# Kernel optimization log

Measured on AMD Instinct MI355X. Metric: run time of the kernel, lower is better.

## Reference

```python
import jax, jax.numpy as jnp
import numpy as np
import math

N_HEAD = 16
N_KV_HEAD = 4
N_EMBD = 2048
HEAD_DIM = N_EMBD // N_HEAD  # 128
SCALE = 1.0 / math.sqrt(HEAD_DIM)
B, T = 2, 2048


def setup_inputs() -> dict:
    key = jax.random.key(0)
    ks = jax.random.split(key, 5)
    s = 0.02
    x = jax.random.normal(ks[0], (B, T, N_EMBD), dtype=jnp.float32)
    wq = jax.random.normal(ks[1], (N_EMBD, N_EMBD), dtype=jnp.float32) * s
    wk = jax.random.normal(ks[2], (N_KV_HEAD * HEAD_DIM, N_EMBD), dtype=jnp.float32) * s
    wv = jax.random.normal(ks[3], (N_KV_HEAD * HEAD_DIM, N_EMBD), dtype=jnp.float32) * s
    wo = jax.random.normal(ks[4], (N_EMBD, N_EMBD), dtype=jnp.float32) * s
    return {"x": x, "wq": wq, "wk": wk, "wv": wv, "wo": wo}


def _forward(x, wq, wk, wv, wo):
    b, t, _ = x.shape
    # Linear layers: y = x @ W.T  (torch Linear weight is (out,in))
    q = (x @ wq.T).reshape(b, t, N_HEAD, HEAD_DIM).transpose(0, 2, 1, 3)      # (B,H,T,D)
    k = (x @ wk.T).reshape(b, t, N_KV_HEAD, HEAD_DIM).transpose(0, 2, 1, 3)  # (B,Hkv,T,D)
    v = (x @ wv.T).reshape(b, t, N_KV_HEAD, HEAD_DIM).transpose(0, 2, 1, 3)
    groups = N_HEAD // N_KV_HEAD
    k = jnp.repeat(k, groups, axis=1)  # repeat_interleave over head dim -> (B,H,T,D)
    v = jnp.repeat(v, groups, axis=1)
    # Causal mask: True above diagonal (masked-out positions)
    mask = jnp.triu(jnp.ones((t, t), dtype=bool), k=1)[None, None]  # (1,1,T,T)
    scores = jnp.einsum('bhqd,bhkd->bhqk', q, k) * SCALE
    scores = jnp.where(mask, -jnp.inf, scores)
    attn = jax.nn.softmax(scores, axis=-1)
    attn = jnp.where(mask, 0.0, attn)
    y = jnp.einsum('bhqk,bhkd->bhqd', attn, v)       # (B,H,T,D)
    y = y.transpose(0, 2, 1, 3).reshape(b, t, N_EMBD)
    return y @ wo.T


def reference(x, wq, wk, wv, wo):
    return _forward(x, wq, wk, wv, wo)
```

## Files before the change

### kernel.cpp

```cpp
#include <hip/hip_runtime.h>
#include <cstdint>
#include <cstddef>

typedef __bf16 bf16_t;
typedef __bf16 bf16x8 __attribute__((ext_vector_type(8)));
typedef __bf16 bf16x4 __attribute__((ext_vector_type(4)));
typedef float f32x4 __attribute__((ext_vector_type(4)));

#define GL2LDS16(gptr, lptr)                                                   \
  __builtin_amdgcn_global_load_lds(                                            \
      (__attribute__((address_space(1))) void*)(gptr),                         \
      (__attribute__((address_space(3))) void*)(lptr), 16, 0, 0)

__device__ __forceinline__ float fast_exp2(float x) {
  float r;
  asm volatile("v_exp_f32 %0, %1" : "=v"(r) : "v"(x));
  return r;
}

#define BATCH 2
#define T_SEQ 2048
#define NH 16
#define NKV 4
#define HD 128
#define EMB 2048
#define KVDIM (NKV * HD)
#define MROWS (BATCH * T_SEQ)

__global__ void cvt_all(const float4* __restrict__ x,  const float4* __restrict__ wq,
                        const float4* __restrict__ wk, const float4* __restrict__ wv,
                        const float4* __restrict__ wo,
                        bf16x4* __restrict__ xb,  bf16x4* __restrict__ wqb,
                        bf16x4* __restrict__ wkb, bf16x4* __restrict__ wvb,
                        bf16x4* __restrict__ wob) {
  const int blk = blockIdx.x;
  const float4* src;
  bf16x4* dst;
  int base;
  if (blk < 8192)       { src = x;  dst = xb;  base = blk; }
  else if (blk < 12288) { src = wq; dst = wqb; base = blk - 8192; }
  else if (blk < 13312) { src = wk; dst = wkb; base = blk - 12288; }
  else if (blk < 14336) { src = wv; dst = wvb; base = blk - 13312; }
  else                  { src = wo; dst = wob; base = blk - 14336; }
  const int i = base * 256 + threadIdx.x;
  const float4 v = src[i];
  dst[i] = bf16x4{(__bf16)v.x, (__bf16)v.y, (__bf16)v.z, (__bf16)v.w};
}

#define BK8 64
#define NT8 (EMB / BK8)

#define LDA(dst, buf, half)                                                    \
  _Pragma("unroll")                                                            \
  for (int i_ = 0; i_ < 4; ++i_) {                                             \
    const int row_ = wm + (half) * 64 + i_ * 16 + l15;                         \
    _Pragma("unroll")                                                          \
    for (int ks_ = 0; ks_ < 2; ++ks_)                                          \
      dst[i_][ks_] = *(const bf16x8*)&(buf)[row_ * 64 +                        \
                                            (((ks_ * 4 + lq) ^ (row_ & 7)) * 8)]; \
  }

#define LDB(dst, buf, qoff)                                                    \
  _Pragma("unroll")                                                            \
  for (int j_ = 0; j_ < 2; ++j_) {                                             \
    const int row_ = 256 + wn + (qoff) + j_ * 16 + l15;                        \
    _Pragma("unroll")                                                          \
    for (int ks_ = 0; ks_ < 2; ++ks_)                                          \
      dst[j_][ks_] = *(const bf16x8*)&(buf)[row_ * 64 +                        \
                                            (((ks_ * 4 + lq) ^ (row_ & 7)) * 8)]; \
  }

#define MM(Af, Bf, ai, bj)                                                     \
  __builtin_amdgcn_s_setprio(1);                                               \
  _Pragma("unroll")                                                            \
  for (int ks_ = 0; ks_ < 2; ++ks_)                                            \
    _Pragma("unroll")                                                          \
    for (int i_ = 0; i_ < 4; ++i_)                                             \
      _Pragma("unroll")                                                        \
      for (int j_ = 0; j_ < 2; ++j_)                                           \
        acc[(ai) + i_][(bj) + j_] = __builtin_amdgcn_mfma_f32_16x16x32_bf16(   \
            Af[i_][ks_], Bf[j_][ks_], acc[(ai) + i_][(bj) + j_], 0, 0, 0);     \
  __builtin_amdgcn_s_setprio(0);

__global__ __launch_bounds__(512, 2)
void gemm_qkv8(const bf16_t* __restrict__ A,
               const bf16_t* __restrict__ Wq, const bf16_t* __restrict__ Wk,
               const bf16_t* __restrict__ Wv,
               bf16_t* __restrict__ Qb, bf16_t* __restrict__ Kb,
               bf16_t* __restrict__ Vt, float qalpha)
{
  __shared__ bf16_t lds0[512 * 64];
  __shared__ bf16_t lds1[512 * 64];

  const int tid  = threadIdx.x;
  const int lane = tid & 63;
  const int wv   = tid >> 6;
  const int l15  = lane & 15;
  const int lq   = lane >> 4;

  const int bid0 = blockIdx.x;
  const int bid  = (bid0 & 7) * 24 + (bid0 >> 3);
  const int mt = bid / 12, nt = bid % 12;
  const int m0 = mt * 256;

  const bf16_t* Bmat; int ncol0, seg;
  if (nt < 8)       { Bmat = Wq; ncol0 = nt * 256;        seg = 0; }
  else if (nt < 10) { Bmat = Wk; ncol0 = (nt - 8) * 256;  seg = 1; }
  else              { Bmat = Wv; ncol0 = (nt - 10) * 256; seg = 2; }

  const int wm = (wv >> 2) * 128;
  const int wn = (wv & 3) * 64;

  f32x4 acc[8][4] = {};

  auto stageAll = [&](bf16_t* dstbuf, int tsrc) {
    const int k0 = tsrc * BK8;
#pragma unroll
    for (int h = 0; h < 4; ++h) {
      const bf16_t* src = (h < 2) ? A : Bmat;
      const int rbase = (h < 2) ? (m0 + h * 128) : (ncol0 + (h - 2) * 128);
      bf16_t* dst = dstbuf + h * 8192;
#pragma unroll
      for (int r = 0; r < 2; ++r) {
        const int c = r * 512 + tid;
        const int row = c >> 3, p = c & 7;
        const int sb = p ^ (row & 7);
        GL2LDS16(src + (size_t)(rbase + row) * EMB + k0 + sb * 8, dst + c * 8);
      }
    }
  };

  stageAll(lds0, 0);
  stageAll(lds1, 1);
  asm volatile("s_waitcnt vmcnt(8)" ::: "memory");
  __builtin_amdgcn_s_barrier();

  bf16x8 a03[4][2], a47[4][2], b01[2][2], b23[2][2];
  LDA(a03, lds0, 0);
  LDB(b01, lds0, 0);

#pragma unroll 1
  for (int t = 0; t < NT8; ++t) {
    bf16_t* curb = (t & 1) ? lds1 : lds0;
    bf16_t* nxtb = (t & 1) ? lds0 : lds1;
    const int tn2 = (t + 2 < NT8) ? t + 2 : NT8 - 1;

    LDB(b23, curb, 32);
    MM(a03, b01, 0, 0);
    __builtin_amdgcn_s_barrier();

    LDA(a47, curb, 1);
    MM(a03, b23, 0, 2);
    asm volatile("s_waitcnt vmcnt(0)" ::: "memory");
    __builtin_amdgcn_s_barrier();

    LDA(a03, nxtb, 0);
    MM(a47, b01, 4, 0);
    __builtin_amdgcn_s_barrier();

    stageAll(curb, tn2);
    LDB(b01, nxtb, 0);
    MM(a47, b23, 4, 2);
    __builtin_amdgcn_s_barrier();
  }
  asm volatile("s_waitcnt vmcnt(0)" ::: "memory");

  if (seg == 0) {
#pragma unroll
    for (int i = 0; i < 8; ++i) {
      const int rbase = m0 + wm + i * 16 + lq * 4;
#pragma unroll
      for (int j = 0; j < 4; ++j) {
        const int col = ncol0 + wn + j * 16 + l15;
#pragma unroll
        for (int r = 0; r < 4; ++r)
          Qb[(size_t)(rbase + r) * EMB + col] = (bf16_t)(acc[i][j][r] * qalpha);
      }
    }
  } else if (seg == 1) {
#pragma unroll
    for (int i = 0; i < 8; ++i) {
      const int rbase = m0 + wm + i * 16 + lq * 4;
#pragma unroll
      for (int j = 0; j < 4; ++j) {
        const int col = ncol0 + wn + j * 16 + l15;
#pragma unroll
        for (int r = 0; r < 4; ++r)
          Kb[(size_t)(rbase + r) * KVDIM + col] = (bf16_t)acc[i][j][r];
      }
    }
  } else {
    const int bb = m0 >> 11;
    const int mloc0 = (m0 & 2047) + wm + lq * 4;
#pragma unroll
    for (int i = 0; i < 8; ++i) {
      const int mloc = mloc0 + i * 16;
#pragma unroll
      for (int j = 0; j < 4; ++j) {
        const int d = ncol0 + wn + j * 16 + l15;
        *(bf16x4*)(Vt + (size_t)(bb * KVDIM + d) * T_SEQ + mloc) =
            bf16x4{(__bf16)acc[i][j][0], (__bf16)acc[i][j][1],
                   (__bf16)acc[i][j][2], (__bf16)acc[i][j][3]};
      }
    }
  }
}

__global__ __launch_bounds__(256, 2)
void gemm_out(const bf16_t* __restrict__ A, const bf16_t* __restrict__ Bm,
              float* __restrict__ C, int M, int N, int K)
{
  __shared__ bf16_t As[128 * 64];
  __shared__ bf16_t Bs[128 * 64];

  const int tid  = threadIdx.x;
  const int lane = tid & 63;
  const int wv   = tid >> 6;
  const int m0 = blockIdx.y * 128;
  const int n0 = blockIdx.x * 128;
  const int wm = (wv >> 1) * 64;
  const int wn = (wv & 1) * 64;
  const int l15 = lane & 15;
  const int lq  = lane >> 4;

  f32x4 acc[4][4] = {};
  const int srow = tid >> 3;
  const int scol = (tid & 7) * 8;

  for (int k0 = 0; k0 < K; k0 += 64) {
#pragma unroll
    for (int r = 0; r < 4; ++r) {
      const int row = r * 32 + srow;
      GL2LDS16(A + (size_t)(m0 + row) * K + k0 + scol, As + row * 64 + scol);
    }
#pragma unroll
    for (int r = 0; r < 4; ++r) {
      const int row = r * 32 + srow;
      GL2LDS16(Bm + (size_t)(n0 + row) * K + k0 + scol, Bs + row * 64 + scol);
    }
    __syncthreads();

#pragma unroll
    for (int ks = 0; ks < 2; ++ks) {
      const int kc = ks * 32 + lq * 8;
      bf16x8 af[4], bf[4];
#pragma unroll
      for (int i = 0; i < 4; ++i)
        af[i] = *(const bf16x8*)(As + (wm + i * 16 + l15) * 64 + kc);
#pragma unroll
      for (int j = 0; j < 4; ++j)
        bf[j] = *(const bf16x8*)(Bs + (wn + j * 16 + l15) * 64 + kc);
#pragma unroll
      for (int i = 0; i < 4; ++i)
#pragma unroll
        for (int j = 0; j < 4; ++j)
          acc[i][j] = __builtin_amdgcn_mfma_f32_16x16x32_bf16(af[i], bf[j], acc[i][j], 0, 0, 0);
    }
    __syncthreads();
  }

#pragma unroll
  for (int i = 0; i < 4; ++i) {
    const int rbase = m0 + wm + i * 16 + lq * 4;
#pragma unroll
    for (int j = 0; j < 4; ++j) {
      const int col = n0 + wn + j * 16 + l15;
#pragma unroll
      for (int r = 0; r < 4; ++r)
        C[(size_t)(rbase + r) * N + col] = acc[i][j][r];
    }
  }
}

#define PSTR 72

__global__ __launch_bounds__(256, 2)
void attn_fwd(const bf16_t* __restrict__ Q, const bf16_t* __restrict__ Kg,
              const bf16_t* __restrict__ Vt, bf16_t* __restrict__ Y)
{
  __shared__ bf16_t Ks[2][64 * 128];
  __shared__ bf16_t Vs[2][128 * 64];
  __shared__ bf16_t Ps[4][16 * PSTR];

  const int tid  = threadIdx.x;
  const int lane = tid & 63;
  const int wv   = tid >> 6;
  const int l15  = lane & 15;
  const int lq   = lane >> 4;
  const int h  = blockIdx.y;
  const int b  = blockIdx.z;
  const int hkv = h >> 2;
  bf16_t* Psw = Ps[wv];

  auto stage = [&](int kt, int bufsel) {
    const int base_t = b * T_SEQ + kt * 64;
#pragma unroll
    for (int r = 0; r < 4; ++r) {
      const int c = r * 256 + tid;
      const int row = c >> 4, p = c & 15;
      const int sb = p ^ (row & 7);
      GL2LDS16(Kg + (size_t)(base_t + row) * KVDIM + hkv * HD + sb * 8,
               &Ks[bufsel][c * 8]);
    }
#pragma unroll
    for (int r = 0; r < 4; ++r) {
      const int c = r * 256 + tid;
      const int row = c >> 3, p = c & 7;
      const int sb = p ^ (row & 7);
      GL2LDS16(Vt + (size_t)(b * KVDIM + hkv * HD + row) * T_SEQ + kt * 64 + sb * 8,
               &Vs[bufsel][c * 8]);
    }
  };

#pragma unroll 1
  for (int ph = 0; ph < 2; ++ph) {
    const int qt = ph ? blockIdx.x : (31 - blockIdx.x);
    const int q0 = qt * 64;
    const int nkt = qt + 1;
    const int qabs = q0 + wv * 16 + l15;

    bf16x8 qf[4];
    {
      const bf16_t* qp = Q + ((size_t)(b * T_SEQ + qabs) * NH + h) * HD + lq * 8;
#pragma unroll
      for (int ds = 0; ds < 4; ++ds)
        qf[ds] = *(const bf16x8*)(qp + ds * 32);
    }

    float l_part = 0.f;
    f32x4 o[8];
#pragma unroll
    for (int nb = 0; nb < 8; ++nb) o[nb] = f32x4{0.f, 0.f, 0.f, 0.f};

    __syncthreads();
    stage(0, 0);

    for (int kt = 0; kt < nkt; ++kt) {
      const int cur = kt & 1;
      __syncthreads();
      if (kt + 1 < nkt) stage(kt + 1, cur ^ 1);

      f32x4 s[4];
#pragma unroll
      for (int nb = 0; nb < 4; ++nb) {
        s[nb] = f32x4{0.f, 0.f, 0.f, 0.f};
        const int row = nb * 16 + l15;
        const int r7  = row & 7;
#pragma unroll
        for (int ds = 0; ds < 4; ++ds) {
          const bf16x8 kf = *(const bf16x8*)&Ks[cur][row * 128 + (((ds * 4 + lq) ^ r7) * 8)];
          s[nb] = __builtin_amdgcn_mfma_f32_16x16x32_bf16(kf, qf[ds], s[nb], 0, 0, 0);
        }
      }

      const bool dia = (kt == nkt - 1);
#pragma unroll
      for (int nb = 0; nb < 4; ++nb) {
        const int kvb = kt * 64 + nb * 16 + lq * 4;
        float p0, p1, p2, p3;
        if (dia) {
          p0 = (kvb + 0 <= qabs) ? fast_exp2(s[nb][0]) : 0.f;
          p1 = (kvb + 1 <= qabs) ? fast_exp2(s[nb][1]) : 0.f;
          p2 = (kvb + 2 <= qabs) ? fast_exp2(s[nb][2]) : 0.f;
          p3 = (kvb + 3 <= qabs) ? fast_exp2(s[nb][3]) : 0.f;
        } else {
          p0 = fast_exp2(s[nb][0]);
          p1 = fast_exp2(s[nb][1]);
          p2 = fast_exp2(s[nb][2]);
          p3 = fast_exp2(s[nb][3]);
        }
        l_part += (p0 + p1) + (p2 + p3);
        *(bf16x4*)(Psw + l15 * PSTR + nb * 16 + lq * 4) =
            bf16x4{(__bf16)p0, (__bf16)p1, (__bf16)p2, (__bf16)p3};
      }

      asm volatile("s_waitcnt lgkmcnt(0)" ::: "memory");

#pragma unroll
      for (int ks = 0; ks < 2; ++ks) {
        const bf16x8 pf = *(const bf16x8*)(Psw + l15 * PSTR + ks * 32 + lq * 8);
#pragma unroll
        for (int nb = 0; nb < 8; ++nb) {
          const int row = nb * 16 + l15;
          const bf16x8 vf = *(const bf16x8*)&Vs[cur][row * 64 + (((ks * 4 + lq) ^ (row & 7)) * 8)];
          o[nb] = __builtin_amdgcn_mfma_f32_16x16x32_bf16(vf, pf, o[nb], 0, 0, 0);
        }
      }
    }

    float lt = l_part;
    lt += __shfl_xor(lt, 16);
    lt += __shfl_xor(lt, 32);
    const float inv = 1.f / lt;
    bf16_t* yp = Y + ((size_t)(b * T_SEQ + qabs) * NH + h) * HD + lq * 4;
#pragma unroll
    for (int nb = 0; nb < 8; ++nb) {
      *(bf16x4*)(yp + nb * 16) = bf16x4{(__bf16)(o[nb][0] * inv), (__bf16)(o[nb][1] * inv),
                                        (__bf16)(o[nb][2] * inv), (__bf16)(o[nb][3] * inv)};
    }
  }
}

extern "C" void kernel_launch(void* const* d_in, const int* in_sizes, int n_in,
                              void* d_out, int out_size, void* d_ws, size_t ws_size,
                              hipStream_t stream) {
  const float* x  = (const float*)d_in[0];
  const float* wq = (const float*)d_in[1];
  const float* wk = (const float*)d_in[2];
  const float* wv = (const float*)d_in[3];
  const float* wo = (const float*)d_in[4];
  float* out = (float*)d_out;

  const size_t n_x  = (size_t)MROWS * EMB;
  const size_t n_wq = (size_t)EMB * EMB;
  const size_t n_wk = (size_t)KVDIM * EMB;

  bf16_t* xb  = (bf16_t*)d_ws;
  bf16_t* wqb = xb  + n_x;
  bf16_t* wkb = wqb + n_wq;
  bf16_t* wvb = wkb + n_wk;
  bf16_t* wob = wvb + n_wk;
  bf16_t* Qb  = wob + n_wq;
  bf16_t* Kb  = Qb + (size_t)MROWS * EMB;
  bf16_t* Vtb = Kb + (size_t)MROWS * KVDIM;
  bf16_t* Yb  = Vtb + (size_t)MROWS * KVDIM;

  dim3 blk(256);

  cvt_all<<<dim3(18432), blk, 0, stream>>>(
      (const float4*)x, (const float4*)wq, (const float4*)wk, (const float4*)wv, (const float4*)wo,
      (bf16x4*)xb, (bf16x4*)wqb, (bf16x4*)wkb, (bf16x4*)wvb, (bf16x4*)wob);

  const float qalpha = 0.08838834764831845f * 1.4426950408889634f;
  gemm_qkv8<<<dim3(192), dim3(512), 0, stream>>>(xb, wqb, wkb, wvb,
                                                 Qb, Kb, Vtb, qalpha);

  attn_fwd<<<dim3(16, NH, BATCH), blk, 0, stream>>>(Qb, Kb, Vtb, Yb);

  gemm_out<<<dim3(EMB / 128, MROWS / 128), blk, 0, stream>>>(Yb, wob, out, MROWS, EMB, EMB);
}
```

Before: 282.4 us.

## Retile fused QKV GEMM to 256x192 tiles for 256 blocks

The fused QKV projection GEMM moves from 256x256 tiles (192 blocks) to 256x192 tiles (256 blocks), so the 3072-wide output splits into 16 column tiles that can straddle the Q/K/V boundaries. This is meant to fill all 256 compute units on the MI355X instead of leaving a quarter idle. Per-chunk weight-row selection is added for loads and per-16-column selection for stores, and the LDS staging and MFMA schedule are reworked with finer-grained half-A and B prefetches. The cost is lower arithmetic intensity per block and more barriers per k-step.

```diff
diff --git a/kernel.cpp b/kernel.cpp
--- a/kernel.cpp
+++ b/kernel.cpp
@@ -49,6 +49,7 @@
 
 #define BK8 64
 #define NT8 (EMB / BK8)
+#define BN 192
 
 #define LDA(dst, buf, half)                                                    \
   _Pragma("unroll")                                                            \
@@ -60,17 +61,26 @@
                                             (((ks_ * 4 + lq) ^ (row_ & 7)) * 8)]; \
   }
 
-#define LDB(dst, buf, qoff)                                                    \
+#define LDB2(dst, buf)                                                         \
   _Pragma("unroll")                                                            \
   for (int j_ = 0; j_ < 2; ++j_) {                                             \
-    const int row_ = 256 + wn + (qoff) + j_ * 16 + l15;                        \
+    const int row_ = 256 + wn + j_ * 16 + l15;                                 \
     _Pragma("unroll")                                                          \
     for (int ks_ = 0; ks_ < 2; ++ks_)                                          \
       dst[j_][ks_] = *(const bf16x8*)&(buf)[row_ * 64 +                        \
                                             (((ks_ * 4 + lq) ^ (row_ & 7)) * 8)]; \
   }
 
-#define MM(Af, Bf, ai, bj)                                                     \
+#define LDB1(dst, buf)                                                         \
+  {                                                                            \
+    const int row_ = 256 + wn + 32 + l15;                                      \
+    _Pragma("unroll")                                                          \
+    for (int ks_ = 0; ks_ < 2; ++ks_)                                          \
+      dst[ks_] = *(const bf16x8*)&(buf)[row_ * 64 +                            \
+                                        (((ks_ * 4 + lq) ^ (row_ & 7)) * 8)];  \
+  }
+
+#define MM16(Af, Bf, ai)                                                       \
   __builtin_amdgcn_s_setprio(1);                                               \
   _Pragma("unroll")                                                            \
   for (int ks_ = 0; ks_ < 2; ++ks_)                                            \
@@ -78,8 +88,18 @@
     for (int i_ = 0; i_ < 4; ++i_)                                             \
       _Pragma("unroll")                                                        \
       for (int j_ = 0; j_ < 2; ++j_)                                           \
-        acc[(ai) + i_][(bj) + j_] = __builtin_amdgcn_mfma_f32_16x16x32_bf16(   \
-            Af[i_][ks_], Bf[j_][ks_], acc[(ai) + i_][(bj) + j_], 0, 0, 0);     \
+        acc[(ai) + i_][j_] = __builtin_amdgcn_mfma_f32_16x16x32_bf16(          \
+            Af[i_][ks_], Bf[j_][ks_], acc[(ai) + i_][j_], 0, 0, 0);            \
+  __builtin_amdgcn_s_setprio(0);
+
+#define MM8(Af, Bf, ai)                                                        \
+  __builtin_amdgcn_s_setprio(1);                                               \
+  _Pragma("unroll")                                                            \
+  for (int ks_ = 0; ks_ < 2; ++ks_)                                            \
+    _Pragma("unroll")                                                          \
+    for (int i_ = 0; i_ < 4; ++i_)                                             \
+      acc[(ai) + i_][2] = __builtin_amdgcn_mfma_f32_16x16x32_bf16(             \
+          Af[i_][ks_], Bf[ks_], acc[(ai) + i_][2], 0, 0, 0);                   \
   __builtin_amdgcn_s_setprio(0);
 
 __global__ __launch_bounds__(512, 2)
@@ -89,8 +109,8 @@
                bf16_t* __restrict__ Qb, bf16_t* __restrict__ Kb,
                bf16_t* __restrict__ Vt, float qalpha)
 {
-  __shared__ bf16_t lds0[512 * 64];
-  __shared__ bf16_t lds1[512 * 64];
+  __shared__ bf16_t lds0[448 * 64];
+  __shared__ bf16_t lds1[448 * 64];
 
   const int tid  = threadIdx.x;
   const int lane = tid & 63;
@@ -99,105 +119,104 @@
   const int lq   = lane >> 4;
 
   const int bid0 = blockIdx.x;
-  const int bid  = (bid0 & 7) * 24 + (bid0 >> 3);
-  const int mt = bid / 12, nt = bid % 12;
+  const int bid  = (bid0 & 7) * 32 + (bid0 >> 3);
+  const int mt = bid >> 4, nt = bid & 15;
   const int m0 = mt * 256;
-
-  const bf16_t* Bmat; int ncol0, seg;
-  if (nt < 8)       { Bmat = Wq; ncol0 = nt * 256;        seg = 0; }
-  else if (nt < 10) { Bmat = Wk; ncol0 = (nt - 8) * 256;  seg = 1; }
-  else              { Bmat = Wv; ncol0 = (nt - 10) * 256; seg = 2; }
+  const int ncol0g = nt * BN;
 
   const int wm = (wv >> 2) * 128;
-  const int wn = (wv & 3) * 64;
-
-  f32x4 acc[8][4] = {};
-
-  auto stageAll = [&](bf16_t* dstbuf, int tsrc) {
+  const int wn = (wv & 3) * 48;
+
+  f32x4 acc[8][3] = {};
+
+  auto stageA_half = [&](bf16_t* dstbuf, int tsrc, int half) {
     const int k0 = tsrc * BK8;
 #pragma unroll
-    for (int h = 0; h < 4; ++h) {
-      const bf16_t* src = (h < 2) ? A : Bmat;
-      const int rbase = (h < 2) ? (m0 + h * 128) : (ncol0 + (h - 2) * 128);
-      bf16_t* dst = dstbuf + h * 8192;
-#pragma unroll
-      for (int r = 0; r < 2; ++r) {
-        const int c = r * 512 + tid;
-        const int row = c >> 3, p = c & 7;
-        const int sb = p ^ (row & 7);
-        GL2LDS16(src + (size_t)(rbase + row) * EMB + k0 + sb * 8, dst + c * 8);
-      }
+    for (int r = 0; r < 2; ++r) {
+      const int c = (half * 2 + r) * 512 + tid;
+      const int row = c >> 3, p = c & 7;
+      const int sb = p ^ (row & 7);
+      GL2LDS16(A + (size_t)(m0 + row) * EMB + k0 + sb * 8, dstbuf + c * 8);
     }
   };
-
-  stageAll(lds0, 0);
-  stageAll(lds1, 1);
-  asm volatile("s_waitcnt vmcnt(8)" ::: "memory");
+  auto stageB = [&](bf16_t* dstbuf, int tsrc) {
+    const int k0 = tsrc * BK8;
+#pragma unroll
+    for (int r = 0; r < 3; ++r) {
+      const int c = r * 512 + tid;
+      const int row = c >> 3, p = c & 7;
+      const int sb = p ^ (row & 7);
+      const int gc = ncol0g + row;
+      const bf16_t* bsrc; int brow;
+      if (gc < EMB)             { bsrc = Wq; brow = gc; }
+      else if (gc < EMB + 512)  { bsrc = Wk; brow = gc - EMB; }
+      else                      { bsrc = Wv; brow = gc - EMB - 512; }
+      GL2LDS16(bsrc + (size_t)brow * EMB + k0 + sb * 8,
+               dstbuf + 256 * 64 + c * 8);
+    }
+  };
+
+  stageA_half(lds0, 0, 0); stageA_half(lds0, 0, 1); stageB(lds0, 0);
+  stageB(lds1, 1); stageA_half(lds1, 1, 0);
+  asm volatile("s_waitcnt vmcnt(5)" ::: "memory");
   __builtin_amdgcn_s_barrier();
 
-  bf16x8 a03[4][2], a47[4][2], b01[2][2], b23[2][2];
-  LDA(a03, lds0, 0);
-  LDB(b01, lds0, 0);
+  bf16x8 a03[4][2], a47[4][2], b01[2][2], b2[2];
 
 #pragma unroll 1
   for (int t = 0; t < NT8; ++t) {
     bf16_t* curb = (t & 1) ? lds1 : lds0;
     bf16_t* nxtb = (t & 1) ? lds0 : lds1;
+    const int tn1 = (t + 1 < NT8) ? t + 1 : NT8 - 1;
     const int tn2 = (t + 2 < NT8) ? t + 2 : NT8 - 1;
 
-    LDB(b23, curb, 32);
-    MM(a03, b01, 0, 0);
+    LDA(a03, curb, 0);
+    LDB2(b01, curb);
+    stageA_half(nxtb, tn1, 1);
+    __builtin_amdgcn_s_barrier();
+    MM16(a03, b01, 0);
+    __builtin_amdgcn_s_barrier();
+
+    LDB1(b2, curb);
+    __builtin_amdgcn_s_barrier();
+    MM8(a03, b2, 0);
     __builtin_amdgcn_s_barrier();
 
     LDA(a47, curb, 1);
-    MM(a03, b23, 0, 2);
-    asm volatile("s_waitcnt vmcnt(0)" ::: "memory");
-    __builtin_amdgcn_s_barrier();
-
-    LDA(a03, nxtb, 0);
-    MM(a47, b01, 4, 0);
-    __builtin_amdgcn_s_barrier();
-
-    stageAll(curb, tn2);
-    LDB(b01, nxtb, 0);
-    MM(a47, b23, 4, 2);
+    stageB(curb, tn2);
+    __builtin_amdgcn_s_barrier();
+    MM8(a47, b2, 4);
+    __builtin_amdgcn_s_barrier();
+
+    stageA_half(curb, tn2, 0);
+    __builtin_amdgcn_s_barrier();
+    MM16(a47, b01, 4);
+    asm volatile("s_waitcnt vmcnt(5)" ::: "memory");
     __builtin_amdgcn_s_barrier();
   }
   asm volatile("s_waitcnt vmcnt(0)" ::: "memory");
 
-  if (seg == 0) {
-#pragma unroll
-    for (int i = 0; i < 8; ++i) {
-      const int rbase = m0 + wm + i * 16 + lq * 4;
-#pragma unroll
-      for (int j = 0; j < 4; ++j) {
-        const int col = ncol0 + wn + j * 16 + l15;
+  const int bb = m0 >> 11;
+  const int mloc0 = (m0 & 2047) + wm + lq * 4;
+#pragma unroll
+  for (int i = 0; i < 8; ++i) {
+    const int rbase = m0 + wm + i * 16 + lq * 4;
+#pragma unroll
+    for (int j = 0; j < 3; ++j) {
+      const int gc0 = ncol0g + wn + j * 16;
+      if (gc0 < EMB) {
+        const int col = gc0 + l15;
 #pragma unroll
         for (int r = 0; r < 4; ++r)
           Qb[(size_t)(rbase + r) * EMB + col] = (bf16_t)(acc[i][j][r] * qalpha);
-      }
-    }
-  } else if (seg == 1) {
-#pragma unroll
-    for (int i = 0; i < 8; ++i) {
-      const int rbase = m0 + wm + i * 16 + lq * 4;
-#pragma unroll
-      for (int j = 0; j < 4; ++j) {
-        const int col = ncol0 + wn + j * 16 + l15;
+      } else if (gc0 < EMB + 512) {
+        const int col = gc0 - EMB + l15;
 #pragma unroll
         for (int r = 0; r < 4; ++r)
           Kb[(size_t)(rbase + r) * KVDIM + col] = (bf16_t)acc[i][j][r];
-      }
-    }
-  } else {
-    const int bb = m0 >> 11;
-    const int mloc0 = (m0 & 2047) + wm + lq * 4;
-#pragma unroll
-    for (int i = 0; i < 8; ++i) {
-      const int mloc = mloc0 + i * 16;
-#pragma unroll
-      for (int j = 0; j < 4; ++j) {
-        const int d = ncol0 + wn + j * 16 + l15;
+      } else {
+        const int d = gc0 - EMB - 512 + l15;
+        const int mloc = mloc0 + i * 16;
         *(bf16x4*)(Vt + (size_t)(bb * KVDIM + d) * T_SEQ + mloc) =
             bf16x4{(__bf16)acc[i][j][0], (__bf16)acc[i][j][1],
                    (__bf16)acc[i][j][2], (__bf16)acc[i][j][3]};
@@ -432,7 +451,7 @@
       (bf16x4*)xb, (bf16x4*)wqb, (bf16x4*)wkb, (bf16x4*)wvb, (bf16x4*)wob);
 
   const float qalpha = 0.08838834764831845f * 1.4426950408889634f;
-  gemm_qkv8<<<dim3(192), dim3(512), 0, stream>>>(xb, wqb, wkb, wvb,
+  gemm_qkv8<<<dim3(256), dim3(512), 0, stream>>>(xb, wqb, wkb, wvb,
                                                  Qb, Kb, Vtb, qalpha);
 
   attn_fwd<<<dim3(16, NH, BATCH), blk, 0, stream>>>(Qb, Kb, Vtb, Yb);
```

New measurement: 273.6 us. 1.03x faster.
